# Kernel optimization log

Hardware: AMD Instinct MI355X
Metric: run time of the kernel (lower is better)

## Reference

```python
import jax, jax.numpy as jnp
import numpy as np

NEG_INF = -1e9  # additive mask value (every row attends to itself, so softmax is safe)


def setup_inputs() -> dict:
    D, H, N = 256, 8, 4096
    key = jax.random.key(0)
    ks = jax.random.split(key, 7)
    slots = jax.random.normal(ks[0], (1, N, D), dtype=jnp.float32)
    batch_idx = jnp.sort(jax.random.randint(ks[1], (N,), 0, 16)).astype(jnp.int32)
    s_in = 1.0 / np.sqrt(D)
    w_in = jax.random.uniform(ks[2], (3 * D, D), jnp.float32, -s_in, s_in)
    b_in = jnp.zeros((3 * D,), jnp.float32)
    w_out = jax.random.uniform(ks[3], (D, D), jnp.float32, -s_in, s_in)
    b_out = jnp.zeros((D,), jnp.float32)
    ln_gamma = jnp.ones((D,), jnp.float32)
    ln_beta = jnp.zeros((D,), jnp.float32)
    return {"slots": slots, "batch_idx": batch_idx, "w_in": w_in, "b_in": b_in,
            "w_out": w_out, "b_out": b_out, "ln_gamma": ln_gamma, "ln_beta": ln_beta}


def _mha_block_diag(x, batch_idx, w_in, b_in, w_out, b_out, num_heads):
    # x: [N, D]
    N, D = x.shape
    hd = D // num_heads
    qkv = x @ w_in.T + b_in                      # [N, 3D]
    q, k, v = jnp.split(qkv, 3, axis=-1)
    q = q.reshape(N, num_heads, hd).transpose(1, 0, 2)   # [H, N, hd]
    k = k.reshape(N, num_heads, hd).transpose(1, 0, 2)
    v = v.reshape(N, num_heads, hd).transpose(1, 0, 2)
    scale = 1.0 / np.sqrt(hd)
    scores = jnp.einsum('hnd,hmd->hnm', q, k) * scale    # [H, N, N]
    mask = batch_idx[:, None] != batch_idx[None, :]      # True = blocked
    scores = jnp.where(mask[None], NEG_INF, scores)
    attn = jax.nn.softmax(scores, axis=-1)
    out = jnp.einsum('hnm,hmd->hnd', attn, v)            # [H, N, hd]
    out = out.transpose(1, 0, 2).reshape(N, D)
    return out @ w_out.T + b_out


def _layer_norm(x, gamma, beta, eps=1e-5):
    mu = jnp.mean(x, axis=-1, keepdims=True)
    var = jnp.mean(jnp.square(x - mu), axis=-1, keepdims=True)
    return (x - mu) * jax.lax.rsqrt(var + eps) * gamma + beta


def reference(slots, batch_idx, w_in, b_in, w_out, b_out, ln_gamma, ln_beta):
    # slots: [1, N, D]; dropout prob is 0.0 (eval-mode reference)
    x = slots[0]
    delta = _mha_block_diag(x, batch_idx, w_in, b_in, w_out, b_out, num_heads=8)
    out = _layer_norm(x + delta, ln_gamma, ln_beta)
    return out[None]
```

## Files before the change

### kernel.cpp

```cpp
#include <hip/hip_runtime.h>
#include <hip/hip_bf16.h>

#define NROWS 4096
#define DMODEL 256
#define NHEADS 8
#define HD 32

typedef __attribute__((ext_vector_type(8))) short short8;
typedef __attribute__((ext_vector_type(4))) float f32x4;

union bf8cast { short8 v; __hip_bfloat16 h[8]; };

__global__ __launch_bounds__(256) void prep_kernel(
    const float* __restrict__ w_in, const int* __restrict__ bidx,
    __hip_bfloat16* __restrict__ Winb, int* __restrict__ segs) {
  const int bid = blockIdx.x;
  if (bid < 192) {
    const int i = (bid * 256 + (int)threadIdx.x) * 4;
    const float4 v = *(const float4*)(w_in + i);
    __hip_bfloat162 lo, hi;
    lo.x = __float2bfloat16(v.x); lo.y = __float2bfloat16(v.y);
    hi.x = __float2bfloat16(v.z); hi.y = __float2bfloat16(v.w);
    *(__hip_bfloat162*)(Winb + i) = lo;
    *(__hip_bfloat162*)(Winb + i + 2) = hi;
  } else {
    const int r = (bid - 192) * 256 + threadIdx.x;
    const int b = bidx[r];
    if (r == 0 || bidx[r - 1] != b) segs[b] = r;
    if (r == NROWS - 1 || bidx[r + 1] != b) segs[16 + b] = r + 1;
  }
}

__global__ __launch_bounds__(256, 4) void gemm_qkv(
    const float* __restrict__ A,
    const __hip_bfloat16* __restrict__ B,
    const float* __restrict__ bias,
    __hip_bfloat16* __restrict__ Qo,
    __hip_bfloat16* __restrict__ Ko,
    __hip_bfloat16* __restrict__ Vo) {
  const int wv   = threadIdx.x >> 6;
  const int lane = threadIdx.x & 63;
  const int lo16 = lane & 15;
  const int quad = lane >> 4;
  const int bm = blockIdx.y * 64 + wv * 16;
  const int bn = blockIdx.x * 64;

  f32x4 acc[4] = {};
  #pragma unroll
  for (int k0 = 0; k0 < 256; k0 += 32) {
    const float4 a0 = *(const float4*)(A + (size_t)(bm + lo16) * 256 + k0 + quad * 8);
    const float4 a1 = *(const float4*)(A + (size_t)(bm + lo16) * 256 + k0 + quad * 8 + 4);
    bf8cast af;
    af.h[0] = __float2bfloat16(a0.x); af.h[1] = __float2bfloat16(a0.y);
    af.h[2] = __float2bfloat16(a0.z); af.h[3] = __float2bfloat16(a0.w);
    af.h[4] = __float2bfloat16(a1.x); af.h[5] = __float2bfloat16(a1.y);
    af.h[6] = __float2bfloat16(a1.z); af.h[7] = __float2bfloat16(a1.w);
    #pragma unroll
    for (int ni = 0; ni < 4; ni++) {
      const short8 bf = *(const short8*)(B + (size_t)(bn + ni * 16 + lo16) * 256 + k0 + quad * 8);
      acc[ni] = __builtin_amdgcn_mfma_f32_16x16x32_bf16(af.v, bf, acc[ni], 0, 0, 0);
    }
  }
  const float scale = 0.17677669529663687f;
  #pragma unroll
  for (int ni = 0; ni < 4; ni++) {
    const int col = bn + ni * 16 + lo16;
    const int sel = col >> 8;
    const int h = (col & 255) >> 5;
    const int d = col & 31;
    const float bv = bias[col];
    #pragma unroll
    for (int r = 0; r < 4; r++) {
      const int n = bm + quad * 4 + r;
      const float v = acc[ni][r] + bv;
      if (sel == 0)      Qo[((size_t)h * NROWS + n) * HD + d] = __float2bfloat16(v * scale);
      else if (sel == 1) Ko[((size_t)h * NROWS + n) * HD + d] = __float2bfloat16(v);
      else               Vo[((size_t)h * HD + d) * NROWS + n] = __float2bfloat16(v);
    }
  }
}

__global__ __launch_bounds__(256, 4) void attn_mfma(
    const __hip_bfloat16* __restrict__ Qb,
    const __hip_bfloat16* __restrict__ Kb,
    const __hip_bfloat16* __restrict__ Vt,
    const int* __restrict__ bidx,
    const int* __restrict__ segs,
    __hip_bfloat16* __restrict__ out)
{
  __shared__ __align__(16) __hip_bfloat16 Plds_all[4][16][40];
  __shared__ float lld[4][16];
  __shared__ float Old[4][16][32];
  const int wv   = threadIdx.x >> 6;
  const int lane = threadIdx.x & 63;
  const int qt   = blockIdx.x >> 3;
  const int h    = blockIdx.x & 7;
  const int r0   = qt * 16;
  const int lo16 = lane & 15;
  const int quad = lane >> 4;
  __hip_bfloat16 (*Plds)[40] = Plds_all[wv];

  int st[4], en[4];
  #pragma unroll
  for (int r = 0; r < 4; r++) {
    const int b = bidx[r0 + quad * 4 + r];
    st[r] = segs[b];
    en[r] = segs[16 + b];
  }
  const int kstart = segs[bidx[r0]] & ~31;
  const int kend   = segs[16 + bidx[r0 + 15]];
  const int ntiles = (kend - kstart + 31) >> 5;

  const short8 qf = *(const short8*)(Qb + ((size_t)h * NROWS + r0 + lo16) * HD + quad * 8);

  f32x4 o0 = {0.f, 0.f, 0.f, 0.f}, o1 = {0.f, 0.f, 0.f, 0.f};
  float l[4] = {0.f, 0.f, 0.f, 0.f};

  for (int t = wv; t < ntiles; t += 4) {
    const int c0 = kstart + t * 32;
    const int col0 = c0 + lo16;
    const int col1 = col0 + 16;
    const int colc0 = min(col0, NROWS - 1);
    const int colc1 = min(col1, NROWS - 1);
    const short8 kf0 = *(const short8*)(Kb + ((size_t)h * NROWS + colc0) * HD + quad * 8);
    const short8 kf1 = *(const short8*)(Kb + ((size_t)h * NROWS + colc1) * HD + quad * 8);
    const int vc = min(c0 + quad * 8, NROWS - 8);
    const short8 vf0 = *(const short8*)(Vt + ((size_t)h * HD + lo16) * NROWS + vc);
    const short8 vf1 = *(const short8*)(Vt + ((size_t)h * HD + 16 + lo16) * NROWS + vc);

    const f32x4 z = {0.f, 0.f, 0.f, 0.f};
    f32x4 s0 = __builtin_amdgcn_mfma_f32_16x16x32_bf16(qf, kf0, z, 0, 0, 0);
    f32x4 s1 = __builtin_amdgcn_mfma_f32_16x16x32_bf16(qf, kf1, z, 0, 0, 0);

    #pragma unroll
    for (int r = 0; r < 4; r++) {
      const bool ok0 = (col0 >= st[r]) & (col0 < en[r]);
      const bool ok1 = (col1 >= st[r]) & (col1 < en[r]);
      const float p0 = ok0 ? __expf(s0[r]) : 0.0f;
      const float p1 = ok1 ? __expf(s1[r]) : 0.0f;
      l[r] += p0 + p1;
      Plds[quad * 4 + r][lo16]      = __float2bfloat16(p0);
      Plds[quad * 4 + r][lo16 + 16] = __float2bfloat16(p1);
    }
    const short8 pf = *(const short8*)&Plds[lo16][quad * 8];
    o0 = __builtin_amdgcn_mfma_f32_16x16x32_bf16(pf, vf0, o0, 0, 0, 0);
    o1 = __builtin_amdgcn_mfma_f32_16x16x32_bf16(pf, vf1, o1, 0, 0, 0);
  }

  #pragma unroll
  for (int r = 0; r < 4; r++) {
    l[r] += __shfl_xor(l[r], 1);
    l[r] += __shfl_xor(l[r], 2);
    l[r] += __shfl_xor(l[r], 4);
    l[r] += __shfl_xor(l[r], 8);
    const int row = quad * 4 + r;
    Old[wv][row][lo16]      = o0[r];
    Old[wv][row][lo16 + 16] = o1[r];
    if (lo16 == 0) lld[wv][row] = l[r];
  }
  __syncthreads();

  const int row = threadIdx.x >> 4;
  const int c   = threadIdx.x & 15;
  float L = 0.f, O0 = 0.f, O1 = 0.f;
  #pragma unroll
  for (int w = 0; w < 4; w++) {
    L  += lld[w][row];
    O0 += Old[w][row][c];
    O1 += Old[w][row][c + 16];
  }
  const float inv = 1.0f / L;
  const int grow = r0 + row;
  out[(size_t)grow * DMODEL + h * HD + c]      = __float2bfloat16(O0 * inv);
  out[(size_t)grow * DMODEL + h * HD + 16 + c] = __float2bfloat16(O1 * inv);
}

__global__ __launch_bounds__(256, 4) void gemm_out_ln(
    const __hip_bfloat16* __restrict__ A,
    const float* __restrict__ B,
    const float* __restrict__ bias,
    const float* __restrict__ x,
    const float* __restrict__ gamma, const float* __restrict__ beta,
    float* __restrict__ out) {
  __shared__ float red1[16][4], red2[16][4];
  const int wv   = threadIdx.x >> 6;
  const int lane = threadIdx.x & 63;
  const int lo16 = lane & 15;
  const int quad = lane >> 4;
  const int r0 = blockIdx.x * 16;
  const int wn = wv * 64;

  f32x4 acc[4] = {};
  #pragma unroll
  for (int k0 = 0; k0 < 256; k0 += 32) {
    const short8 af = *(const short8*)(A + (size_t)(r0 + lo16) * 256 + k0 + quad * 8);
    #pragma unroll
    for (int ni = 0; ni < 4; ni++) {
      const float4 b0 = *(const float4*)(B + (size_t)(wn + ni * 16 + lo16) * 256 + k0 + quad * 8);
      const float4 b1 = *(const float4*)(B + (size_t)(wn + ni * 16 + lo16) * 256 + k0 + quad * 8 + 4);
      bf8cast bf;
      bf.h[0] = __float2bfloat16(b0.x); bf.h[1] = __float2bfloat16(b0.y);
      bf.h[2] = __float2bfloat16(b0.z); bf.h[3] = __float2bfloat16(b0.w);
      bf.h[4] = __float2bfloat16(b1.x); bf.h[5] = __float2bfloat16(b1.y);
      bf.h[6] = __float2bfloat16(b1.z); bf.h[7] = __float2bfloat16(b1.w);
      acc[ni] = __builtin_amdgcn_mfma_f32_16x16x32_bf16(af, bf.v, acc[ni], 0, 0, 0);
    }
  }

  float val[4][4];
  float s1[4] = {}, s2[4] = {};
  #pragma unroll
  for (int ni = 0; ni < 4; ni++) {
    const int col = wn + ni * 16 + lo16;
    const float bv = bias[col];
    #pragma unroll
    for (int r = 0; r < 4; r++) {
      const int row = r0 + quad * 4 + r;
      const float v = acc[ni][r] + bv + x[(size_t)row * DMODEL + col];
      val[ni][r] = v;
      s1[r] += v;
      s2[r] += v * v;
    }
  }
  #pragma unroll
  for (int r = 0; r < 4; r++) {
    #pragma unroll
    for (int off = 1; off < 16; off <<= 1) {
      s1[r] += __shfl_xor(s1[r], off);
      s2[r] += __shfl_xor(s2[r], off);
    }
    if (lo16 == 0) { red1[quad * 4 + r][wv] = s1[r]; red2[quad * 4 + r][wv] = s2[r]; }
  }
  __syncthreads();
  #pragma unroll
  for (int r = 0; r < 4; r++) {
    const int lrow = quad * 4 + r;
    const float mean = (red1[lrow][0] + red1[lrow][1] + red1[lrow][2] + red1[lrow][3]) * (1.0f / DMODEL);
    const float ex2  = (red2[lrow][0] + red2[lrow][1] + red2[lrow][2] + red2[lrow][3]) * (1.0f / DMODEL);
    const float rstd = rsqrtf(fmaxf(ex2 - mean * mean, 0.0f) + 1e-5f);
    const int row = r0 + lrow;
    #pragma unroll
    for (int ni = 0; ni < 4; ni++) {
      const int col = wn + ni * 16 + lo16;
      out[(size_t)row * DMODEL + col] =
          (val[ni][r] - mean) * rstd * gamma[col] + beta[col];
    }
  }
}

extern "C" void kernel_launch(void* const* d_in, const int* in_sizes, int n_in,
                              void* d_out, int out_size, void* d_ws, size_t ws_size,
                              hipStream_t stream) {
  const float* slots  = (const float*)d_in[0];
  const int*   bidx   = (const int*)  d_in[1];
  const float* w_in   = (const float*)d_in[2];
  const float* b_in   = (const float*)d_in[3];
  const float* w_out  = (const float*)d_in[4];
  const float* b_out  = (const float*)d_in[5];
  const float* ln_g   = (const float*)d_in[6];
  const float* ln_b   = (const float*)d_in[7];
  float* out = (float*)d_out;

  char* ws = (char*)d_ws;
  __hip_bfloat16* Qb    = (__hip_bfloat16*)(ws);
  __hip_bfloat16* Kb    = (__hip_bfloat16*)(ws + (2u << 20));
  __hip_bfloat16* Vt    = (__hip_bfloat16*)(ws + (4u << 20));
  __hip_bfloat16* attnb = (__hip_bfloat16*)(ws + (6u << 20));
  __hip_bfloat16* Winb  = (__hip_bfloat16*)(ws + (8u << 20));
  int*            segs  = (int*)           (ws + (9u << 20));

  prep_kernel<<<208, 256, 0, stream>>>(w_in, bidx, Winb, segs);
  {
    dim3 grid(768 / 64, NROWS / 64);
    gemm_qkv<<<grid, 256, 0, stream>>>(slots, Winb, b_in, Qb, Kb, Vt);
  }
  attn_mfma<<<(NROWS / 16) * NHEADS, 256, 0, stream>>>(Qb, Kb, Vt, bidx,
                                                       segs, attnb);
  gemm_out_ln<<<NROWS / 16, 256, 0, stream>>>(attnb, w_out, b_out, slots,
                                              ln_g, ln_b, out);
}
```

Baseline: 115.3 us.

## Fuse attention with output projection and LayerNorm in one kernel

Merges the attention kernel and the output GEMM+LayerNorm kernel. Each 512-thread block handles 16 rows, with one wave per head. Each wave now walks all key tiles of its segment instead of splitting them across four waves, so the cross-wave partial reduction goes away. The normalized attention output is staged in LDS as bf16 and consumed directly by the output projection, which removes the global round trip for attnb and one launch. The cost is per-head serial work over the whole key range within each wave and a 2048-block grid becoming 256 larger blocks, which lowers parallelism.

New measurement: 116.9 us. Within noise of the previous version (+1.4%).

```diff
diff --git a/kernel.cpp b/kernel.cpp
--- a/kernel.cpp
+++ b/kernel.cpp
@@ -80,124 +80,98 @@
   }
 }
 
-__global__ __launch_bounds__(256, 4) void attn_mfma(
+__global__ __launch_bounds__(512, 2) void attn_out_ln(
     const __hip_bfloat16* __restrict__ Qb,
     const __hip_bfloat16* __restrict__ Kb,
     const __hip_bfloat16* __restrict__ Vt,
     const int* __restrict__ bidx,
     const int* __restrict__ segs,
-    __hip_bfloat16* __restrict__ out)
-{
-  __shared__ __align__(16) __hip_bfloat16 Plds_all[4][16][40];
-  __shared__ float lld[4][16];
-  __shared__ float Old[4][16][32];
-  const int wv   = threadIdx.x >> 6;
-  const int lane = threadIdx.x & 63;
-  const int qt   = blockIdx.x >> 3;
-  const int h    = blockIdx.x & 7;
-  const int r0   = qt * 16;
-  const int lo16 = lane & 15;
-  const int quad = lane >> 4;
-  __hip_bfloat16 (*Plds)[40] = Plds_all[wv];
-
-  int st[4], en[4];
-  #pragma unroll
-  for (int r = 0; r < 4; r++) {
-    const int b = bidx[r0 + quad * 4 + r];
-    st[r] = segs[b];
-    en[r] = segs[16 + b];
-  }
-  const int kstart = segs[bidx[r0]] & ~31;
-  const int kend   = segs[16 + bidx[r0 + 15]];
-  const int ntiles = (kend - kstart + 31) >> 5;
-
-  const short8 qf = *(const short8*)(Qb + ((size_t)h * NROWS + r0 + lo16) * HD + quad * 8);
-
-  f32x4 o0 = {0.f, 0.f, 0.f, 0.f}, o1 = {0.f, 0.f, 0.f, 0.f};
-  float l[4] = {0.f, 0.f, 0.f, 0.f};
-
-  for (int t = wv; t < ntiles; t += 4) {
-    const int c0 = kstart + t * 32;
-    const int col0 = c0 + lo16;
-    const int col1 = col0 + 16;
-    const int colc0 = min(col0, NROWS - 1);
-    const int colc1 = min(col1, NROWS - 1);
-    const short8 kf0 = *(const short8*)(Kb + ((size_t)h * NROWS + colc0) * HD + quad * 8);
-    const short8 kf1 = *(const short8*)(Kb + ((size_t)h * NROWS + colc1) * HD + quad * 8);
-    const int vc = min(c0 + quad * 8, NROWS - 8);
-    const short8 vf0 = *(const short8*)(Vt + ((size_t)h * HD + lo16) * NROWS + vc);
-    const short8 vf1 = *(const short8*)(Vt + ((size_t)h * HD + 16 + lo16) * NROWS + vc);
-
-    const f32x4 z = {0.f, 0.f, 0.f, 0.f};
-    f32x4 s0 = __builtin_amdgcn_mfma_f32_16x16x32_bf16(qf, kf0, z, 0, 0, 0);
-    f32x4 s1 = __builtin_amdgcn_mfma_f32_16x16x32_bf16(qf, kf1, z, 0, 0, 0);
-
-    #pragma unroll
-    for (int r = 0; r < 4; r++) {
-      const bool ok0 = (col0 >= st[r]) & (col0 < en[r]);
-      const bool ok1 = (col1 >= st[r]) & (col1 < en[r]);
-      const float p0 = ok0 ? __expf(s0[r]) : 0.0f;
-      const float p1 = ok1 ? __expf(s1[r]) : 0.0f;
-      l[r] += p0 + p1;
-      Plds[quad * 4 + r][lo16]      = __float2bfloat16(p0);
-      Plds[quad * 4 + r][lo16 + 16] = __float2bfloat16(p1);
-    }
-    const short8 pf = *(const short8*)&Plds[lo16][quad * 8];
-    o0 = __builtin_amdgcn_mfma_f32_16x16x32_bf16(pf, vf0, o0, 0, 0, 0);
-    o1 = __builtin_amdgcn_mfma_f32_16x16x32_bf16(pf, vf1, o1, 0, 0, 0);
-  }
-
-  #pragma unroll
-  for (int r = 0; r < 4; r++) {
-    l[r] += __shfl_xor(l[r], 1);
-    l[r] += __shfl_xor(l[r], 2);
-    l[r] += __shfl_xor(l[r], 4);
-    l[r] += __shfl_xor(l[r], 8);
-    const int row = quad * 4 + r;
-    Old[wv][row][lo16]      = o0[r];
-    Old[wv][row][lo16 + 16] = o1[r];
-    if (lo16 == 0) lld[wv][row] = l[r];
-  }
-  __syncthreads();
-
-  const int row = threadIdx.x >> 4;
-  const int c   = threadIdx.x & 15;
-  float L = 0.f, O0 = 0.f, O1 = 0.f;
-  #pragma unroll
-  for (int w = 0; w < 4; w++) {
-    L  += lld[w][row];
-    O0 += Old[w][row][c];
-    O1 += Old[w][row][c + 16];
-  }
-  const float inv = 1.0f / L;
-  const int grow = r0 + row;
-  out[(size_t)grow * DMODEL + h * HD + c]      = __float2bfloat16(O0 * inv);
-  out[(size_t)grow * DMODEL + h * HD + 16 + c] = __float2bfloat16(O1 * inv);
-}
-
-__global__ __launch_bounds__(256, 4) void gemm_out_ln(
-    const __hip_bfloat16* __restrict__ A,
-    const float* __restrict__ B,
-    const float* __restrict__ bias,
+    const float* __restrict__ Wout,
+    const float* __restrict__ b_out,
     const float* __restrict__ x,
     const float* __restrict__ gamma, const float* __restrict__ beta,
-    float* __restrict__ out) {
-  __shared__ float red1[16][4], red2[16][4];
+    float* __restrict__ out)
+{
+  __shared__ __align__(16) __hip_bfloat16 Plds_all[8][16][40];
+  __shared__ __align__(16) __hip_bfloat16 Alds[16][264];
+  __shared__ float red1[16][8], red2[16][8];
   const int wv   = threadIdx.x >> 6;
   const int lane = threadIdx.x & 63;
   const int lo16 = lane & 15;
   const int quad = lane >> 4;
-  const int r0 = blockIdx.x * 16;
-  const int wn = wv * 64;
-
-  f32x4 acc[4] = {};
+  const int r0   = blockIdx.x * 16;
+  __hip_bfloat16 (*Plds)[40] = Plds_all[wv];
+
+  {
+    const int h = wv;
+    int st[4], en[4];
+    #pragma unroll
+    for (int r = 0; r < 4; r++) {
+      const int b = bidx[r0 + quad * 4 + r];
+      st[r] = segs[b];
+      en[r] = segs[16 + b];
+    }
+    const int kstart = segs[bidx[r0]] & ~31;
+    const int kend   = segs[16 + bidx[r0 + 15]];
+
+    const short8 qf = *(const short8*)(Qb + ((size_t)h * NROWS + r0 + lo16) * HD + quad * 8);
+
+    f32x4 o0 = {0.f, 0.f, 0.f, 0.f}, o1 = {0.f, 0.f, 0.f, 0.f};
+    float l[4] = {0.f, 0.f, 0.f, 0.f};
+
+    for (int c0 = kstart; c0 < kend; c0 += 32) {
+      const int col0 = c0 + lo16;
+      const int col1 = col0 + 16;
+      const int colc0 = min(col0, NROWS - 1);
+      const int colc1 = min(col1, NROWS - 1);
+      const short8 kf0 = *(const short8*)(Kb + ((size_t)h * NROWS + colc0) * HD + quad * 8);
+      const short8 kf1 = *(const short8*)(Kb + ((size_t)h * NROWS + colc1) * HD + quad * 8);
+      const int vc = min(c0 + quad * 8, NROWS - 8);
+      const short8 vf0 = *(const short8*)(Vt + ((size_t)h * HD + lo16) * NROWS + vc);
+      const short8 vf1 = *(const short8*)(Vt + ((size_t)h * HD + 16 + lo16) * NROWS + vc);
+
+      const f32x4 z = {0.f, 0.f, 0.f, 0.f};
+      f32x4 s0 = __builtin_amdgcn_mfma_f32_16x16x32_bf16(qf, kf0, z, 0, 0, 0);
+      f32x4 s1 = __builtin_amdgcn_mfma_f32_16x16x32_bf16(qf, kf1, z, 0, 0, 0);
+
+      #pragma unroll
+      for (int r = 0; r < 4; r++) {
+        const bool ok0 = (col0 >= st[r]) & (col0 < en[r]);
+        const bool ok1 = (col1 >= st[r]) & (col1 < en[r]);
+        const float p0 = ok0 ? __expf(s0[r]) : 0.0f;
+        const float p1 = ok1 ? __expf(s1[r]) : 0.0f;
+        l[r] += p0 + p1;
+        Plds[quad * 4 + r][lo16]      = __float2bfloat16(p0);
+        Plds[quad * 4 + r][lo16 + 16] = __float2bfloat16(p1);
+      }
+      const short8 pf = *(const short8*)&Plds[lo16][quad * 8];
+      o0 = __builtin_amdgcn_mfma_f32_16x16x32_bf16(pf, vf0, o0, 0, 0, 0);
+      o1 = __builtin_amdgcn_mfma_f32_16x16x32_bf16(pf, vf1, o1, 0, 0, 0);
+    }
+
+    #pragma unroll
+    for (int r = 0; r < 4; r++) {
+      l[r] += __shfl_xor(l[r], 1);
+      l[r] += __shfl_xor(l[r], 2);
+      l[r] += __shfl_xor(l[r], 4);
+      l[r] += __shfl_xor(l[r], 8);
+      const float inv = 1.0f / l[r];
+      const int row = quad * 4 + r;
+      Alds[row][h * HD + lo16]      = __float2bfloat16(o0[r] * inv);
+      Alds[row][h * HD + 16 + lo16] = __float2bfloat16(o1[r] * inv);
+    }
+  }
+  __syncthreads();
+
+  f32x4 acc[2] = {};
   #pragma unroll
   for (int k0 = 0; k0 < 256; k0 += 32) {
-    const short8 af = *(const short8*)(A + (size_t)(r0 + lo16) * 256 + k0 + quad * 8);
-    #pragma unroll
-    for (int ni = 0; ni < 4; ni++) {
-      const float4 b0 = *(const float4*)(B + (size_t)(wn + ni * 16 + lo16) * 256 + k0 + quad * 8);
-      const float4 b1 = *(const float4*)(B + (size_t)(wn + ni * 16 + lo16) * 256 + k0 + quad * 8 + 4);
+    const short8 af = *(const short8*)&Alds[lo16][k0 + quad * 8];
+    #pragma unroll
+    for (int ni = 0; ni < 2; ni++) {
+      const int bc = wv * 32 + ni * 16 + lo16;
+      const float4 b0 = *(const float4*)(Wout + (size_t)bc * 256 + k0 + quad * 8);
+      const float4 b1 = *(const float4*)(Wout + (size_t)bc * 256 + k0 + quad * 8 + 4);
       bf8cast bf;
       bf.h[0] = __float2bfloat16(b0.x); bf.h[1] = __float2bfloat16(b0.y);
       bf.h[2] = __float2bfloat16(b0.z); bf.h[3] = __float2bfloat16(b0.w);
@@ -207,12 +181,12 @@
     }
   }
 
-  float val[4][4];
+  float val[2][4];
   float s1[4] = {}, s2[4] = {};
   #pragma unroll
-  for (int ni = 0; ni < 4; ni++) {
-    const int col = wn + ni * 16 + lo16;
-    const float bv = bias[col];
+  for (int ni = 0; ni < 2; ni++) {
+    const int col = wv * 32 + ni * 16 + lo16;
+    const float bv = b_out[col];
     #pragma unroll
     for (int r = 0; r < 4; r++) {
       const int row = r0 + quad * 4 + r;
@@ -235,13 +209,16 @@
   #pragma unroll
   for (int r = 0; r < 4; r++) {
     const int lrow = quad * 4 + r;
-    const float mean = (red1[lrow][0] + red1[lrow][1] + red1[lrow][2] + red1[lrow][3]) * (1.0f / DMODEL);
-    const float ex2  = (red2[lrow][0] + red2[lrow][1] + red2[lrow][2] + red2[lrow][3]) * (1.0f / DMODEL);
+    float t1 = 0.f, t2 = 0.f;
+    #pragma unroll
+    for (int w = 0; w < 8; w++) { t1 += red1[lrow][w]; t2 += red2[lrow][w]; }
+    const float mean = t1 * (1.0f / DMODEL);
+    const float ex2  = t2 * (1.0f / DMODEL);
     const float rstd = rsqrtf(fmaxf(ex2 - mean * mean, 0.0f) + 1e-5f);
     const int row = r0 + lrow;
     #pragma unroll
-    for (int ni = 0; ni < 4; ni++) {
-      const int col = wn + ni * 16 + lo16;
+    for (int ni = 0; ni < 2; ni++) {
+      const int col = wv * 32 + ni * 16 + lo16;
       out[(size_t)row * DMODEL + col] =
           (val[ni][r] - mean) * rstd * gamma[col] + beta[col];
     }
@@ -262,20 +239,18 @@
   float* out = (float*)d_out;
 
   char* ws = (char*)d_ws;
-  __hip_bfloat16* Qb    = (__hip_bfloat16*)(ws);
-  __hip_bfloat16* Kb    = (__hip_bfloat16*)(ws + (2u << 20));
-  __hip_bfloat16* Vt    = (__hip_bfloat16*)(ws + (4u << 20));
-  __hip_bfloat16* attnb = (__hip_bfloat16*)(ws + (6u << 20));
-  __hip_bfloat16* Winb  = (__hip_bfloat16*)(ws + (8u << 20));
-  int*            segs  = (int*)           (ws + (9u << 20));
+  __hip_bfloat16* Qb   = (__hip_bfloat16*)(ws);
+  __hip_bfloat16* Kb   = (__hip_bfloat16*)(ws + (2u << 20));
+  __hip_bfloat16* Vt   = (__hip_bfloat16*)(ws + (4u << 20));
+  __hip_bfloat16* Winb = (__hip_bfloat16*)(ws + (6u << 20));
+  int*            segs = (int*)           (ws + (7u << 20));
 
   prep_kernel<<<208, 256, 0, stream>>>(w_in, bidx, Winb, segs);
   {
     dim3 grid(768 / 64, NROWS / 64);
     gemm_qkv<<<grid, 256, 0, stream>>>(slots, Winb, b_in, Qb, Kb, Vt);
   }
-  attn_mfma<<<(NROWS / 16) * NHEADS, 256, 0, stream>>>(Qb, Kb, Vt, bidx,
-                                                       segs, attnb);
-  gemm_out_ln<<<NROWS / 16, 256, 0, stream>>>(attnb, w_out, b_out, slots,
+  attn_out_ln<<<NROWS / 16, 512, 0, stream>>>(Qb, Kb, Vt, bidx, segs,
+                                              w_out, b_out, slots,
                                               ln_g, ln_b, out);
 }
```
